# Optimization experiments

Hardware: AMD Instinct MI355X
Metric: run time of the kernel (lower is better)

## Reference

```python
import jax, jax.numpy as jnp
import numpy as np

B, S, D = 2, 2048, 2048
HQ, HKV = 32, 8
DH = D // HQ  # 64
NUM_REP = HQ // HKV  # 4


def setup_inputs() -> dict:
    key = jax.random.key(0)
    k1, k2, k3, k4, k5 = jax.random.split(key, 5)
    scale = 0.02
    return {
        "x": jax.random.normal(k1, (B, S, D), dtype=jnp.float32),
        "Wq": jax.random.normal(k2, (D, HQ * DH), dtype=jnp.float32) * scale,
        "Wk": jax.random.normal(k3, (D, HKV * DH), dtype=jnp.float32) * scale,
        "Wv": jax.random.normal(k4, (D, HKV * DH), dtype=jnp.float32) * scale,
        "Wo": jax.random.normal(k5, (HQ * DH, D), dtype=jnp.float32) * scale,
    }


def reference(x, Wq, Wk, Wv, Wo):
    b, s, _ = x.shape
    # projections
    xq = (x @ Wq).reshape(b, s, HQ, DH)    # [B,S,HQ,DH]
    xk = (x @ Wk).reshape(b, s, HKV, DH)   # [B,S,HKV,DH]
    xv = (x @ Wv).reshape(b, s, HKV, DH)
    # repeat kv heads to match query heads (GQA expand)
    keys = jnp.repeat(xk, NUM_REP, axis=2)    # [B,S,HQ,DH]
    values = jnp.repeat(xv, NUM_REP, axis=2)
    # scores: [B,HQ,S,S], fp32 softmax (no causal mask in original)
    scores = jnp.einsum("bqhd,bkhd->bhqk", xq, keys) / jnp.sqrt(jnp.float32(DH))
    probs = jax.nn.softmax(scores.astype(jnp.float32), axis=-1).astype(xq.dtype)
    context = jnp.einsum("bhqk,bkhd->bqhd", probs, values)  # [B,S,HQ,DH]
    context = context.reshape(b, s, HQ * DH)
    return context @ Wo
```

## Files before the change

kernel.cpp:

```cpp
#include <hip/hip_runtime.h>
#include <cstdint>
#include <cstddef>
#include <cmath>

typedef __bf16 bf16x8 __attribute__((ext_vector_type(8)));
typedef float  f32x4  __attribute__((ext_vector_type(4)));
typedef unsigned short us4 __attribute__((ext_vector_type(4)));
typedef unsigned short us2 __attribute__((ext_vector_type(2)));

__device__ __forceinline__ unsigned short f2bf(float f) {
    union { float f; unsigned int u; } v; v.f = f;
    unsigned int u = v.u;
    u += 0x7fffu + ((u >> 16) & 1u);
    return (unsigned short)(u >> 16);
}

__device__ __forceinline__ unsigned int fbits(float f) {
    union { float f; unsigned int u; } v; v.f = f; return v.u;
}

__device__ __forceinline__ unsigned int pk_bf16_trunc(float a, float b) {
    return __builtin_amdgcn_perm(fbits(b), fbits(a), 0x07060302u);
}

__device__ __forceinline__ void gld_lds16(const void* g, void* l) {
    __builtin_amdgcn_global_load_lds((__attribute__((address_space(1))) void*)g,
                                     (__attribute__((address_space(3))) void*)l,
                                     16, 0, 0);
}

#define BB   2
#define SS   2048
#define DD   2048
#define HQ   32
#define HKV  8
#define DH   64
#define MM   (BB * SS)
#define NQKV 3072

#define QSCALE 0.18033688011112042f

__global__ __launch_bounds__(256) void prep(const float* __restrict__ x,
                                            const float* __restrict__ Wq,
                                            const float* __restrict__ Wk,
                                            const float* __restrict__ Wv,
                                            const float* __restrict__ Wo,
                                            unsigned short* __restrict__ xb,
                                            unsigned short* __restrict__ WqkvT,
                                            unsigned short* __restrict__ WoT) {
    const int bid = blockIdx.x;
    if (bid < 8192) {
        const int i = (bid * 256 + threadIdx.x) * 4;
        const float4 f = *(const float4*)(x + i);
        us4 o;
        o[0] = f2bf(f.x); o[1] = f2bf(f.y); o[2] = f2bf(f.z); o[3] = f2bf(f.w);
        *(us4*)(xb + i) = o;
        return;
    }
    const float* src; unsigned short* dst; int C, bx, by; float scl = 1.0f;
    int r = bid - 8192;
    if (r < 2048) {
        src = Wq; dst = WqkvT; C = 2048; bx = r & 63; by = r >> 6; scl = QSCALE;
    } else if (r < 4096) {
        r -= 2048; src = Wo; dst = WoT; C = 2048; bx = r & 63; by = r >> 6;
    } else if (r < 4608) {
        r -= 4096; src = Wk; dst = WqkvT + (size_t)2048 * 2048; C = 512; bx = r & 15; by = r >> 4;
    } else {
        r -= 4608; src = Wv; dst = WqkvT + (size_t)2560 * 2048; C = 512; bx = r & 15; by = r >> 4;
    }
    const int R = 2048;
    __shared__ __attribute__((aligned(16))) float tile[64][33];
    const int c0 = bx * 32, r0 = by * 64;
    const int tx = threadIdx.x & 31, ty = threadIdx.x >> 5;
    #pragma unroll
    for (int dy = 0; dy < 64; dy += 8)
        tile[ty + dy][tx] = src[(size_t)(r0 + ty + dy) * C + c0 + tx];
    __syncthreads();
    #pragma unroll
    for (int dc = 0; dc < 32; dc += 8) {
        const int c = ty + dc;
        us2 o;
        o[0] = f2bf(tile[2 * tx][c] * scl);
        o[1] = f2bf(tile[2 * tx + 1][c] * scl);
        *(us2*)(dst + (size_t)(c0 + c) * R + r0 + 2 * tx) = o;
    }
}

__global__ __launch_bounds__(256) void transpose_v(const unsigned short* __restrict__ qkv,
                                                   unsigned short* __restrict__ vt) {
    __shared__ __attribute__((aligned(16))) unsigned short tile[32][33];
    const int s0 = blockIdx.x * 32, d0 = blockIdx.y * 32;
    const int bh = blockIdx.z;
    const int b = bh >> 3, kvh = bh & 7;
    const int tx = threadIdx.x & 31, ty = threadIdx.x >> 5;
    #pragma unroll
    for (int dy = 0; dy < 32; dy += 8)
        tile[ty + dy][tx] =
            qkv[(size_t)(b * SS + s0 + ty + dy) * NQKV + 2560 + kvh * DH + d0 + tx];
    __syncthreads();
    #pragma unroll
    for (int dy = 0; dy < 32; dy += 8)
        vt[(size_t)((b * HKV + kvh) * DH + d0 + ty + dy) * SS + s0 + tx] =
            tile[tx][ty + dy];
}

__global__ __launch_bounds__(512, 2) void gemm192(const unsigned short* __restrict__ A,
                                                  const unsigned short* __restrict__ Bt,
                                                  unsigned short* __restrict__ Cout,
                                                  int M, int N, int K) {
    __shared__ __attribute__((aligned(16))) unsigned short As[2][256 * 64];
    __shared__ __attribute__((aligned(16))) unsigned short Bs[2][192 * 64];
    const int lid = blockIdx.x;
    const int bm = ((lid & 7) << 1) | ((lid >> 3) & 1);
    const int bn = lid >> 4;
    const int tid = threadIdx.x;
    const int wv = tid >> 6, lane = tid & 63;
    const int wm = (wv >> 2) * 128;
    const int wn = (wv & 3) * 48;
    const int g = lane >> 4, l15 = lane & 15;
    const int sr = lane >> 3;
    const int sc8 = ((lane & 7) ^ (sr & 7)) * 8;
    const int r7 = l15 & 7;

    f32x4 acc[8][3] = {};
    const unsigned short* spA[4];
    const unsigned short* spB[3];
    #pragma unroll
    for (int j = 0; j < 4; ++j)
        spA[j] = A + (size_t)(bm * 256 + (wv * 4 + j) * 8 + sr) * K + sc8;
    #pragma unroll
    for (int j = 0; j < 3; ++j)
        spB[j] = Bt + (size_t)(bn * 192 + wv * 24 + j * 8 + sr) * K + sc8;

    #define GSTAGE(BUF)                                                       \
        do {                                                                  \
            _Pragma("unroll")                                                 \
            for (int j = 0; j < 4; ++j) {                                     \
                gld_lds16(spA[j], &As[BUF][(wv * 4 + j) * 512]);              \
                spA[j] += 64;                                                 \
            }                                                                 \
            _Pragma("unroll")                                                 \
            for (int j = 0; j < 3; ++j) {                                     \
                gld_lds16(spB[j], &Bs[BUF][(wv * 3 + j) * 512]);              \
                spB[j] += 64;                                                 \
            }                                                                 \
        } while (0)

    #define GCOMPUTE(BUF)                                                     \
        do {                                                                  \
            const unsigned short* as = As[BUF];                               \
            const unsigned short* bs = Bs[BUF];                               \
            bf16x8 bfr[3][2];                                                 \
            _Pragma("unroll")                                                 \
            for (int n = 0; n < 3; ++n)                                       \
                _Pragma("unroll")                                             \
                for (int ks = 0; ks < 2; ++ks)                                \
                    bfr[n][ks] = *(const bf16x8*)&bs[(wn + n * 16 + l15) * 64 \
                                                 + ((ks * 4 + g) ^ r7) * 8];  \
            _Pragma("unroll")                                                 \
            for (int q = 0; q < 4; ++q) {                                     \
                bf16x8 af[2][2];                                              \
                _Pragma("unroll")                                             \
                for (int mi = 0; mi < 2; ++mi)                                \
                    _Pragma("unroll")                                         \
                    for (int ks = 0; ks < 2; ++ks)                            \
                        af[mi][ks] = *(const bf16x8*)&as[                     \
                            (wm + (q * 2 + mi) * 16 + l15) * 64               \
                            + ((ks * 4 + g) ^ r7) * 8];                       \
                _Pragma("unroll")                                             \
                for (int ks = 0; ks < 2; ++ks)                                \
                    _Pragma("unroll")                                         \
                    for (int mi = 0; mi < 2; ++mi)                            \
                        _Pragma("unroll")                                     \
                        for (int n = 0; n < 3; ++n)                           \
                            acc[q * 2 + mi][n] =                              \
                                __builtin_amdgcn_mfma_f32_16x16x32_bf16(      \
                                    af[mi][ks], bfr[n][ks],                   \
                                    acc[q * 2 + mi][n], 0, 0, 0);             \
            }                                                                 \
        } while (0)

    GSTAGE(0);
    GSTAGE(1);
    asm volatile("s_waitcnt vmcnt(7)" ::: "memory");
    __builtin_amdgcn_s_barrier();

    #pragma unroll 1
    for (int t2 = 0; t2 < 16; ++t2) {
        GCOMPUTE(0);
        __builtin_amdgcn_s_barrier();
        if (t2 < 15) {
            GSTAGE(0);
            asm volatile("s_waitcnt vmcnt(7)" ::: "memory");
        } else {
            asm volatile("s_waitcnt vmcnt(0)" ::: "memory");
        }
        __builtin_amdgcn_s_barrier();
        GCOMPUTE(1);
        if (t2 == 15) break;
        __builtin_amdgcn_s_barrier();
        GSTAGE(1);
        asm volatile("s_waitcnt vmcnt(7)" ::: "memory");
        __builtin_amdgcn_s_barrier();
    }

    #pragma unroll
    for (int i = 0; i < 8; ++i) {
        #pragma unroll
        for (int n = 0; n < 3; ++n) {
            const int col = bn * 192 + wn + n * 16 + l15;
            #pragma unroll
            for (int r = 0; r < 4; ++r) {
                const int row = bm * 256 + wm + i * 16 + g * 4 + r;
                Cout[(size_t)row * N + col] = f2bf(acc[i][n][r]);
            }
        }
    }
    #undef GSTAGE
    #undef GCOMPUTE
}

template <int OUT_BF16>
__global__ __launch_bounds__(256) void gemm_bt(const unsigned short* __restrict__ A,
                                               const unsigned short* __restrict__ Bt,
                                               void* __restrict__ Cout,
                                               int M, int N, int K) {
    __shared__ __attribute__((aligned(16))) unsigned short As[128 * 64];
    __shared__ __attribute__((aligned(16))) unsigned short Bs[128 * 64];
    const int bm = blockIdx.x, bn = blockIdx.y;
    const int tid = threadIdx.x;
    const int wave = tid >> 6, lane = tid & 63;
    const int wm = (wave >> 1) * 64, wn = (wave & 1) * 64;
    const int g = lane >> 4, l15 = lane & 15;
    const int sr = lane >> 3;
    const int sc8 = ((lane & 7) ^ (sr & 7)) * 8;
    const int r7 = l15 & 7;

    f32x4 acc[4][4] = {};
    const unsigned short* aBase = A  + (size_t)(bm * 128) * K;
    const unsigned short* bBase = Bt + (size_t)(bn * 128) * K;

    for (int kt = 0; kt < K; kt += 64) {
        __syncthreads();
        #pragma unroll
        for (int j = 0; j < 4; ++j) {
            const int i = wave * 4 + j;
            gld_lds16(aBase + (size_t)(i * 8 + sr) * K + kt + sc8, &As[i * 512]);
            gld_lds16(bBase + (size_t)(i * 8 + sr) * K + kt + sc8, &Bs[i * 512]);
        }
        __syncthreads();
        #pragma unroll
        for (int ks = 0; ks < 2; ++ks) {
            bf16x8 af[4], bfr[4];
            #pragma unroll
            for (int t = 0; t < 4; ++t) {
                af[t]  = *(const bf16x8*)&As[(wm + t * 16 + l15) * 64 + ((ks * 4 + g) ^ r7) * 8];
                bfr[t] = *(const bf16x8*)&Bs[(wn + t * 16 + l15) * 64 + ((ks * 4 + g) ^ r7) * 8];
            }
            #pragma unroll
            for (int i = 0; i < 4; ++i)
                #pragma unroll
                for (int j = 0; j < 4; ++j)
                    acc[i][j] = __builtin_amdgcn_mfma_f32_16x16x32_bf16(
                        af[i], bfr[j], acc[i][j], 0, 0, 0);
        }
    }
    #pragma unroll
    for (int i = 0; i < 4; ++i) {
        #pragma unroll
        for (int j = 0; j < 4; ++j) {
            const int col = bn * 128 + wn + j * 16 + l15;
            #pragma unroll
            for (int r = 0; r < 4; ++r) {
                const int row = bm * 128 + wm + i * 16 + g * 4 + r;
                const float v = acc[i][j][r];
                if (OUT_BF16)
                    ((unsigned short*)Cout)[(size_t)row * N + col] = f2bf(v);
                else
                    ((float*)Cout)[(size_t)row * N + col] = v;
            }
        }
    }
}

__global__ __launch_bounds__(256, 4) void flash_attn(const unsigned short* __restrict__ qkv,
                                                     const unsigned short* __restrict__ vt,
                                                     unsigned short* __restrict__ ctx) {
    __shared__ __attribute__((aligned(16))) unsigned short Ks[2][64 * 64];
    __shared__ __attribute__((aligned(16))) unsigned short Vs[2][64 * 64];

    const int qt = blockIdx.x, h = blockIdx.y, b = blockIdx.z;
    const int kvh = h >> 2;
    const int tid = threadIdx.x, wave = tid >> 6, lane = tid & 63;
    const int g = lane >> 4, l15 = lane & 15;
    const int sr = lane >> 3;
    const int sc8 = ((lane & 7) ^ (sr & 7)) * 8;
    const int r7 = l15 & 7;
    const int qb = qt * 128 + wave * 32;

    const unsigned short* kbase = qkv + (size_t)(b * SS) * NQKV + 2048 + kvh * DH;
    const unsigned short* vbase = vt + (size_t)((b * HKV + kvh) * DH) * SS;

    bf16x8 qf[2][2];
    #pragma unroll
    for (int n = 0; n < 2; ++n)
        #pragma unroll
        for (int kh = 0; kh < 2; ++kh)
            qf[n][kh] = *(const bf16x8*)(qkv +
                (size_t)(b * SS + qb + n * 16 + l15) * NQKV + h * DH + kh * 32 + g * 8);

    bf16x8 ones;
    #pragma unroll
    for (int i = 0; i < 8; ++i) ones[i] = (__bf16)1.0f;

    const f32x4 z4 = {0.0f, 0.0f, 0.0f, 0.0f};

    const unsigned short* sp[4];
    size_t sadv;
    if (wave < 2) {
        #pragma unroll
        for (int j = 0; j < 4; ++j) {
            const int rho = (wave * 4 + j) * 8 + sr;
            const int key = (rho & 0x23) | ((rho & 0x0C) << 1) | ((rho & 0x10) >> 2);
            sp[j] = kbase + (size_t)key * NQKV + sc8;
        }
        sadv = (size_t)64 * NQKV;
    } else {
        #pragma unroll
        for (int j = 0; j < 4; ++j)
            sp[j] = vbase + (size_t)(((wave - 2) * 4 + j) * 8 + sr) * SS + sc8;
        sadv = 64;
    }

    #define STAGE(buf)                                                        \
        do {                                                                  \
            if (wave < 2) {                                                   \
                _Pragma("unroll")                                             \
                for (int j = 0; j < 4; ++j)                                   \
                    gld_lds16(sp[j], &Ks[buf][(wave * 4 + j) * 512]);         \
            } else {                                                          \
                _Pragma("unroll")                                             \
                for (int j = 0; j < 4; ++j)                                   \
                    gld_lds16(sp[j], &Vs[buf][((wave - 2) * 4 + j) * 512]);   \
            }                                                                 \
            _Pragma("unroll")                                                 \
            for (int j = 0; j < 4; ++j) sp[j] += sadv;                        \
        } while (0)

    f32x4 oacc[2][4] = {};
    f32x4 lacc[2] = {};

    #define TILE(BUF)                                                                          \
        do {                                                                                   \
            const unsigned short* ks = Ks[BUF];                                                \
            const unsigned short* vs = Vs[BUF];                                                \
            _Pragma("unroll")                                                                  \
            for (int p = 0; p < 2; ++p) {                                                      \
                uint4 pk4[2];                                                                  \
                _Pragma("unroll")                                                              \
                for (int hh = 0; hh < 2; ++hh) {                                               \
                    const int t = 2 * p + hh;                                                  \
                    bf16x8 kf0 = *(const bf16x8*)&ks[(t * 16 + l15) * 64 + ((g) ^ r7) * 8];    \
                    bf16x8 kf1 = *(const bf16x8*)&ks[(t * 16 + l15) * 64 + ((4 + g) ^ r7) * 8];\
                    _Pragma("unroll")                                                          \
                    for (int n = 0; n < 2; ++n) {                                              \
                        f32x4 c = __builtin_amdgcn_mfma_f32_16x16x32_bf16(                     \
                            kf0, qf[n][0], z4, 0, 0, 0);                                       \
                        c = __builtin_amdgcn_mfma_f32_16x16x32_bf16(                           \
                            kf1, qf[n][1], c, 0, 0, 0);                                        \
                        f32x4 pe;                                                              \
                        pe[0] = __builtin_amdgcn_exp2f(c[0]);                                  \
                        pe[1] = __builtin_amdgcn_exp2f(c[1]);                                  \
                        pe[2] = __builtin_amdgcn_exp2f(c[2]);                                  \
                        pe[3] = __builtin_amdgcn_exp2f(c[3]);                                  \
                        const unsigned int lo = pk_bf16_trunc(pe[0], pe[1]);                   \
                        const unsigned int hi = pk_bf16_trunc(pe[2], pe[3]);                   \
                        if (hh == 0) { pk4[n].x = lo; pk4[n].y = hi; }                         \
                        else         { pk4[n].z = lo; pk4[n].w = hi; }                         \
                    }                                                                          \
                }                                                                              \
                __builtin_amdgcn_s_setprio(1);                                                 \
                _Pragma("unroll")                                                              \
                for (int nt = 0; nt < 4; ++nt) {                                               \
                    bf16x8 vf = *(const bf16x8*)&vs[(nt * 16 + l15) * 64 +                     \
                                                    (((p << 2) + g) ^ r7) * 8];                \
                    _Pragma("unroll")                                                          \
                    for (int m = 0; m < 2; ++m) {                                              \
                        union { uint4 u; bf16x8 v; } pa; pa.u = pk4[m];                        \
                        oacc[m][nt] = __builtin_amdgcn_mfma_f32_16x16x32_bf16(                 \
                            pa.v, vf, oacc[m][nt], 0, 0, 0);                                   \
                        if (nt == 0)                                                           \
                            lacc[m] = __builtin_amdgcn_mfma_f32_16x16x32_bf16(                 \
                                pa.v, ones, lacc[m], 0, 0, 0);                                 \
                    }                                                                          \
                }                                                                              \
                __builtin_amdgcn_s_setprio(0);                                                 \
            }                                                                                  \
        } while (0)

    STAGE(0);

    #pragma unroll 1
    for (int kt2 = 0; kt2 < 16; ++kt2) {
        __syncthreads();
        STAGE(1);
        TILE(0);
        __syncthreads();
        if (kt2 < 15) STAGE(0);
        TILE(1);
    }

    #pragma unroll
    for (int m = 0; m < 2; ++m) {
        #pragma unroll
        for (int r = 0; r < 4; ++r) {
            const float inv = __builtin_amdgcn_rcpf(lacc[m][r]);
            const int token = b * SS + qb + m * 16 + g * 4 + r;
            #pragma unroll
            for (int nt = 0; nt < 4; ++nt)
                ctx[(size_t)token * (HQ * DH) + h * DH + nt * 16 + l15] =
                    f2bf(oacc[m][nt][r] * inv);
        }
    }
    #undef TILE
    #undef STAGE
}

extern "C" void kernel_launch(void* const* d_in, const int* in_sizes, int n_in,
                              void* d_out, int out_size, void* d_ws, size_t ws_size,
                              hipStream_t stream) {
    (void)in_sizes; (void)n_in; (void)out_size; (void)ws_size;
    const float* x  = (const float*)d_in[0];
    const float* Wq = (const float*)d_in[1];
    const float* Wk = (const float*)d_in[2];
    const float* Wv = (const float*)d_in[3];
    const float* Wo = (const float*)d_in[4];
    float* out = (float*)d_out;

    char* ws = (char*)d_ws;
    unsigned short* xb     = (unsigned short*)(ws);
    unsigned short* WqkvT  = (unsigned short*)(ws + 16777216);
    unsigned short* WoT    = (unsigned short*)(ws + 29360128);
    unsigned short* QKV    = (unsigned short*)(ws + 37748736);
    unsigned short* Vt     = (unsigned short*)(ws + 62914560);
    unsigned short* ctx    = (unsigned short*)(ws + 67108864);

    prep<<<13312, 256, 0, stream>>>(x, Wq, Wk, Wv, Wo, xb, WqkvT, WoT);

    gemm192<<<256, 512, 0, stream>>>(xb, WqkvT, QKV, MM, NQKV, DD);

    transpose_v<<<dim3(64, 2, 16), 256, 0, stream>>>(QKV, Vt);

    flash_attn<<<dim3(16, 32, 2), 256, 0, stream>>>(QKV, Vt, ctx);

    gemm_bt<0><<<dim3(32, 16), 256, 0, stream>>>(ctx, WoT, out, MM, DD, DD);
}
```

Before: 276.2 us.

## Replace output projection GEMM with 256x128 tiled triple-buffered kernel

Swaps the 128x128-tile output projection GEMM for a new kernel using 256x128 tiles, 512 threads and a three-stage async global-to-LDS pipeline with block-index swizzling. The larger tile raises data reuse per block, the deeper pipeline hides load latency, and the grid drops to 256 blocks, roughly one per CU. In exchange it uses more LDS and registers, which may limit occupancy, and the fixed loop count assumes K is 2048.

```diff
diff --git a/kernel.cpp b/kernel.cpp
--- a/kernel.cpp
+++ b/kernel.cpp
@@ -218,6 +218,122 @@
     }
     #undef GSTAGE
     #undef GCOMPUTE
+}
+
+__global__ __launch_bounds__(512, 2) void gemm128o3(const unsigned short* __restrict__ A,
+                                                    const unsigned short* __restrict__ Bt,
+                                                    float* __restrict__ Cout,
+                                                    int M, int N, int K) {
+    __shared__ __attribute__((aligned(16))) unsigned short As[3][256 * 64];
+    __shared__ __attribute__((aligned(16))) unsigned short Bs[3][128 * 64];
+    const int lid = blockIdx.x;
+    const int bm = ((lid & 7) << 1) | ((lid >> 3) & 1);
+    const int bn = lid >> 4;
+    const int tid = threadIdx.x;
+    const int wv = tid >> 6, lane = tid & 63;
+    const int wm = (wv >> 2) * 128;
+    const int wn = (wv & 3) * 32;
+    const int g = lane >> 4, l15 = lane & 15;
+    const int sr = lane >> 3;
+    const int sc8 = ((lane & 7) ^ (sr & 7)) * 8;
+    const int r7 = l15 & 7;
+
+    f32x4 acc[8][2] = {};
+    const unsigned short* spA[4];
+    const unsigned short* spB[2];
+    #pragma unroll
+    for (int j = 0; j < 4; ++j)
+        spA[j] = A + (size_t)(bm * 256 + (wv * 4 + j) * 8 + sr) * K + sc8;
+    #pragma unroll
+    for (int j = 0; j < 2; ++j)
+        spB[j] = Bt + (size_t)(bn * 128 + wv * 16 + j * 8 + sr) * K + sc8;
+
+    #define OSTAGE(AP, BP)                                                    \
+        do {                                                                  \
+            _Pragma("unroll")                                                 \
+            for (int j = 0; j < 4; ++j) {                                     \
+                gld_lds16(spA[j], (AP) + (wv * 4 + j) * 512);                 \
+                spA[j] += 64;                                                 \
+            }                                                                 \
+            _Pragma("unroll")                                                 \
+            for (int j = 0; j < 2; ++j) {                                     \
+                gld_lds16(spB[j], (BP) + (wv * 2 + j) * 512);                 \
+                spB[j] += 64;                                                 \
+            }                                                                 \
+        } while (0)
+
+    #define OCOMPUTE(AP, BP)                                                  \
+        do {                                                                  \
+            const unsigned short* as = (AP);                                  \
+            const unsigned short* bs = (BP);                                  \
+            bf16x8 bfr[2][2];                                                 \
+            _Pragma("unroll")                                                 \
+            for (int n = 0; n < 2; ++n)                                       \
+                _Pragma("unroll")                                             \
+                for (int ks = 0; ks < 2; ++ks)                                \
+                    bfr[n][ks] = *(const bf16x8*)&bs[(wn + n * 16 + l15) * 64 \
+                                                 + ((ks * 4 + g) ^ r7) * 8];  \
+            _Pragma("unroll")                                                 \
+            for (int q = 0; q < 4; ++q) {                                     \
+                bf16x8 af[2][2];                                              \
+                _Pragma("unroll")                                             \
+                for (int mi = 0; mi < 2; ++mi)                                \
+                    _Pragma("unroll")                                         \
+                    for (int ks = 0; ks < 2; ++ks)                            \
+                        af[mi][ks] = *(const bf16x8*)&as[                     \
+                            (wm + (q * 2 + mi) * 16 + l15) * 64               \
+                            + ((ks * 4 + g) ^ r7) * 8];                       \
+                _Pragma("unroll")                                             \
+                for (int ks = 0; ks < 2; ++ks)                                \
+                    _Pragma("unroll")                                         \
+                    for (int mi = 0; mi < 2; ++mi)                            \
+                        _Pragma("unroll")                                     \
+                        for (int n = 0; n < 2; ++n)                           \
+                            acc[q * 2 + mi][n] =                              \
+                                __builtin_amdgcn_mfma_f32_16x16x32_bf16(      \
+                                    af[mi][ks], bfr[n][ks],                   \
+                                    acc[q * 2 + mi][n], 0, 0, 0);             \
+            }                                                                 \
+        } while (0)
+
+    OSTAGE(As[0], Bs[0]);
+    OSTAGE(As[1], Bs[1]);
+    OSTAGE(As[2], Bs[2]);
+    asm volatile("s_waitcnt vmcnt(12)" ::: "memory");
+    __builtin_amdgcn_s_barrier();
+
+    int cur = 0;
+    #pragma unroll 1
+    for (int t = 0; t < 32; ++t) {
+        OCOMPUTE(As[cur], Bs[cur]);
+        if (t == 31) break;
+        __builtin_amdgcn_s_barrier();
+        if (t < 29) {
+            OSTAGE(As[cur], Bs[cur]);
+            asm volatile("s_waitcnt vmcnt(12)" ::: "memory");
+        } else if (t == 29) {
+            asm volatile("s_waitcnt vmcnt(6)" ::: "memory");
+        } else {
+            asm volatile("s_waitcnt vmcnt(0)" ::: "memory");
+        }
+        __builtin_amdgcn_s_barrier();
+        cur = (cur == 2) ? 0 : cur + 1;
+    }
+
+    #pragma unroll
+    for (int i = 0; i < 8; ++i) {
+        #pragma unroll
+        for (int n = 0; n < 2; ++n) {
+            const int col = bn * 128 + wn + n * 16 + l15;
+            #pragma unroll
+            for (int r = 0; r < 4; ++r) {
+                const int row = bm * 256 + wm + i * 16 + g * 4 + r;
+                Cout[(size_t)row * N + col] = acc[i][n][r];
+            }
+        }
+    }
+    #undef OSTAGE
+    #undef OCOMPUTE
 }
 
 template <int OUT_BF16>
@@ -453,5 +569,5 @@
 
     flash_attn<<<dim3(16, 32, 2), 256, 0, stream>>>(QKV, Vt, ctx);
 
-    gemm_bt<0><<<dim3(32, 16), 256, 0, stream>>>(ctx, WoT, out, MM, DD, DD);
-}
+    gemm128o3<<<256, 512, 0, stream>>>(ctx, WoT, out, MM, DD, DD);
+}
```

After: 298.7 us. +8.1%, slower.
